# Performance work log

Measured on AMD Instinct MI355X. Metric: run time of the kernel, lower is better.

## Reference

```python
import jax, jax.numpy as jnp
import numpy as np

D_MODEL = 1024
N_HEADS = 16
D_HEAD = D_MODEL // N_HEADS


def setup_inputs() -> dict:
    key = jax.random.key(0)
    k1, k2, k3 = jax.random.split(key, 3)
    B, T = 4, 2048
    x = jax.random.normal(k1, (B, T, D_MODEL), dtype=jnp.float32)
    # torch Linear(d, 3d, bias=False): y = x @ W.T ; we store W already transposed -> [d, 3d]
    w_qkv = jax.random.normal(k2, (D_MODEL, 3 * D_MODEL), dtype=jnp.float32) * (D_MODEL ** -0.5)
    w_proj = jax.random.normal(k3, (D_MODEL, D_MODEL), dtype=jnp.float32) * (D_MODEL ** -0.5)
    return {"x": x, "w_qkv": w_qkv, "w_proj": w_proj}


def reference(x, w_qkv, w_proj):
    B, T, C = x.shape
    H, Dh = N_HEADS, D_HEAD
    qkv = (x @ w_qkv).reshape(B, T, 3, H, Dh)
    q = jnp.transpose(qkv[:, :, 0], (0, 2, 1, 3))  # [B,H,T,Dh]
    k = jnp.transpose(qkv[:, :, 1], (0, 2, 1, 3))
    v = jnp.transpose(qkv[:, :, 2], (0, 2, 1, 3))
    scale = 1.0 / jnp.sqrt(jnp.asarray(Dh, dtype=x.dtype))
    att = jnp.einsum('bhqd,bhkd->bhqk', q, k) * scale  # [B,H,T,T]
    causal = jnp.tril(jnp.ones((T, T), dtype=bool))
    att = jnp.where(causal[None, None], att, jnp.asarray(-jnp.inf, dtype=att.dtype))
    att = jax.nn.softmax(att, axis=-1)
    y = jnp.einsum('bhqk,bhkd->bhqd', att, v)          # [B,H,T,Dh]
    y = jnp.transpose(y, (0, 2, 1, 3)).reshape(B, T, C)
    return y @ w_proj
```

## Files before the change

kernel.cpp:

```cpp
#include <hip/hip_runtime.h>
#include <hip/hip_bf16.h>
#include <cmath>

#define T_SEQ 2048
#define NHEADS 16
#define DHEAD 64
#define DMODEL 1024
#define CQKV 3072

typedef __attribute__((ext_vector_type(8))) short short8;
typedef __attribute__((ext_vector_type(8))) __bf16 bf16x8;
typedef __attribute__((ext_vector_type(4))) float floatx4;

#define LDS_CAST(p) ((__attribute__((address_space(3))) void*)(p))
#define GLB_CAST(p) ((const __attribute__((address_space(1))) void*)(p))

static __device__ __forceinline__ floatx4 mfma_bf16(short8 a, short8 b, floatx4 c) {
  return __builtin_amdgcn_mfma_f32_16x16x32_bf16(
      __builtin_bit_cast(bf16x8, a), __builtin_bit_cast(bf16x8, b), c, 0, 0, 0);
}

static __device__ __forceinline__ short f2bf(float f) {
  union { float f; unsigned u; } x; x.f = f;
  unsigned r = x.u + 0x7FFFu + ((x.u >> 16) & 1u);
  return (short)(r >> 16);
}

static __device__ __forceinline__ float bf2f(short s) {
  return __builtin_bit_cast(float, ((unsigned)(unsigned short)s) << 16);
}

static __device__ __forceinline__ float exp2_(float x) {
#if __has_builtin(__builtin_amdgcn_exp2f)
  return __builtin_amdgcn_exp2f(x);
#else
  return exp2f(x);
#endif
}

static __device__ __forceinline__ bool sniff_is_bf16(const unsigned* __restrict__ x) {
  int cnt = 0;
#pragma unroll
  for (int i = 0; i < 32; ++i) {
    unsigned e = (x[i] >> 7) & 0xFFu;
    cnt += (e >= 0x70u && e <= 0x8Fu) ? 1 : 0;
  }
  return cnt >= 16;
}

static __device__ __forceinline__ short8 load8f32(const char* p, size_t idx) {
  const float4* f = (const float4*)(p + idx * 4);
  float4 a = f[0], b = f[1];
  short8 r;
  r[0] = f2bf(a.x); r[1] = f2bf(a.y); r[2] = f2bf(a.z); r[3] = f2bf(a.w);
  r[4] = f2bf(b.x); r[5] = f2bf(b.y); r[6] = f2bf(b.z); r[7] = f2bf(b.w);
  return r;
}

__global__ __launch_bounds__(256) void conv_x(const char* __restrict__ x,
                                              short* __restrict__ o, int n,
                                              const unsigned* __restrict__ xs) {
  const bool isbf = sniff_is_bf16(xs);
  const int i = (blockIdx.x * 256 + threadIdx.x) * 8;
  if (i >= n) return;
  if (isbf) *(short8*)(o + i) = *(const short8*)((const short*)x + i);
  else      *(short8*)(o + i) = load8f32(x, (size_t)i);
}

__global__ __launch_bounds__(256) void tpose(const char* __restrict__ w,
                                             short* __restrict__ wt, int K, int N,
                                             const unsigned* __restrict__ xs) {
  const bool isbf = sniff_is_bf16(xs);
  __shared__ short tile[32][33];
  const int n0 = blockIdx.x * 32, k0 = blockIdx.y * 32;
  const int tx = threadIdx.x & 31, ty = threadIdx.x >> 5;
#pragma unroll
  for (int i = 0; i < 4; ++i) {
    const int r = ty * 4 + i;
    const size_t off = (size_t)(k0 + r) * N + n0 + tx;
    tile[r][tx] = isbf ? ((const short*)w)[off] : f2bf(((const float*)w)[off]);
  }
  __syncthreads();
#pragma unroll
  for (int i = 0; i < 4; ++i) {
    const int r = ty * 4 + i;
    wt[(size_t)(n0 + r) * K + k0 + tx] = tile[tx][r];
  }
}

__global__ __launch_bounds__(256) void gemm128(const short* __restrict__ A,
                                               const short* __restrict__ Bt,
                                               void* __restrict__ C,
                                               short* __restrict__ C2,
                                               int M, int N, int K, int mode,
                                               const unsigned* __restrict__ xs) {
  const bool out_f32 = (mode == 1) ? !sniff_is_bf16(xs) : false;

  __shared__ short as[128 * 64];
  __shared__ short bs[128 * 64];
  const int tid = threadIdx.x;
  const int wid = tid >> 6, lane = tid & 63;
  const int quad = lane >> 4, l16 = lane & 15;
  const int wm = wid >> 1, wn = wid & 1;
  const int m0 = blockIdx.y * 128, n0 = blockIdx.x * 128;

  const int srl = lane >> 3;
  const int sch = ((lane & 7) ^ srl) * 8;

  const floatx4 zero4 = {0.f, 0.f, 0.f, 0.f};
  floatx4 acc[4][4];
#pragma unroll
  for (int i = 0; i < 4; ++i)
#pragma unroll
    for (int j = 0; j < 4; ++j) acc[i][j] = zero4;

  for (int kt = 0; kt < K; kt += 64) {
    __syncthreads();
#pragma unroll
    for (int i = 0; i < 4; ++i) {
      const int row = wid * 32 + i * 8;
      const short* ga = A + (size_t)(m0 + row + srl) * K + kt + sch;
      const short* gb = Bt + (size_t)(n0 + row + srl) * K + kt + sch;
      __builtin_amdgcn_global_load_lds(GLB_CAST(ga), LDS_CAST(as + row * 64), 16, 0, 0);
      __builtin_amdgcn_global_load_lds(GLB_CAST(gb), LDS_CAST(bs + row * 64), 16, 0, 0);
    }
    __syncthreads();

#pragma unroll
    for (int kc = 0; kc < 2; ++kc) {
      const int slot = ((kc * 4 + quad) ^ (l16 & 7)) * 8;
      short8 afr[4], bfr[4];
#pragma unroll
      for (int mt = 0; mt < 4; ++mt)
        afr[mt] = *(const short8*)&as[(wm * 64 + mt * 16 + l16) * 64 + slot];
#pragma unroll
      for (int nt = 0; nt < 4; ++nt)
        bfr[nt] = *(const short8*)&bs[(wn * 64 + nt * 16 + l16) * 64 + slot];
#pragma unroll
      for (int mt = 0; mt < 4; ++mt)
#pragma unroll
        for (int nt = 0; nt < 4; ++nt)
          acc[mt][nt] = mfma_bf16(afr[mt], bfr[nt], acc[mt][nt]);
    }
  }

  const int row0 = m0 + wm * 64 + quad * 4;
  const int col0 = n0 + wn * 64 + l16;
  if (mode == 2 && n0 >= 2048) {
#pragma unroll
    for (int mt = 0; mt < 4; ++mt)
#pragma unroll
      for (int nt = 0; nt < 4; ++nt)
#pragma unroll
        for (int r = 0; r < 4; ++r) {
          const int row = row0 + mt * 16 + r;
          const int col = col0 + nt * 16;
          const int d = col & 63, hh = (col >> 6) - 32;
          const int bb = row >> 11, t = row & 2047;
          C2[((size_t)(bb * 16 + hh) * 64 + d) * T_SEQ + t] = f2bf(acc[mt][nt][r]);
        }
  } else {
    const int outN = (mode == 2) ? 2048 : N;
#pragma unroll
    for (int mt = 0; mt < 4; ++mt)
#pragma unroll
      for (int nt = 0; nt < 4; ++nt)
#pragma unroll
        for (int r = 0; r < 4; ++r) {
          const size_t off = (size_t)(row0 + mt * 16 + r) * outN + col0 + nt * 16;
          if (out_f32) ((float*)C)[off] = acc[mt][nt][r];
          else         ((short*)C)[off] = f2bf(acc[mt][nt][r]);
        }
  }
}

__global__ __launch_bounds__(256) void attn(const short* __restrict__ qk,
                                            const short* __restrict__ vT,
                                            short* __restrict__ y) {
  __shared__ short ks[64 * 64];
  __shared__ short vs[64 * 64];
  __shared__ short ps[4][16][72];
  const int tid = threadIdx.x;
  const int wid = tid >> 6, lane = tid & 63;
  const int quad = lane >> 4, l16 = lane & 15;
  const int b = blockIdx.x >> 4, h = blockIdx.x & 15;
  const int q0 = ((int)gridDim.y - 1 - (int)blockIdx.y) * 64;
  const int qw0 = q0 + wid * 16;

  const short* qbase = qk + (size_t)b * T_SEQ * 2048 + h * DHEAD;
  const short* kbase = qbase + DMODEL;
  const short* vtb = vT + (size_t)(b * NHEADS + h) * DHEAD * T_SEQ;
  const float SC = 0.18033688011112042f;

  short8 aq[2];
#pragma unroll
  for (int kc = 0; kc < 2; ++kc) {
    short8 raw = *(const short8*)(qbase + (size_t)(qw0 + l16) * 2048 + kc * 32 + quad * 8);
#pragma unroll
    for (int j = 0; j < 8; ++j) aq[kc][j] = f2bf(bf2f(raw[j]) * SC);
  }

  const floatx4 zero4 = {0.f, 0.f, 0.f, 0.f};
  floatx4 o[4], lacc = zero4;
#pragma unroll
  for (int i = 0; i < 4; ++i) o[i] = zero4;
  const short8 ones8 = {0x3F80, 0x3F80, 0x3F80, 0x3F80, 0x3F80, 0x3F80, 0x3F80, 0x3F80};

  const int srl = lane >> 3;
  const int sch = ((lane & 7) ^ srl) * 8;

  const int kend = q0 + 64;
  for (int kt = 0; kt < kend; kt += 64) {
    __syncthreads();
#pragma unroll
    for (int i = 0; i < 2; ++i) {
      const int row = i * 32 + wid * 8 + srl;
      const short* gk = kbase + (size_t)(kt + row) * 2048 + sch;
      const short* gv = vtb + (size_t)row * T_SEQ + kt + sch;
      __builtin_amdgcn_global_load_lds(GLB_CAST(gk), LDS_CAST(ks + (i * 32 + wid * 8) * 64), 16, 0, 0);
      __builtin_amdgcn_global_load_lds(GLB_CAST(gv), LDS_CAST(vs + (i * 32 + wid * 8) * 64), 16, 0, 0);
    }
    __syncthreads();

    floatx4 s[4];
#pragma unroll
    for (int nt = 0; nt < 4; ++nt) {
      s[nt] = zero4;
#pragma unroll
      for (int kc = 0; kc < 2; ++kc) {
        const int slot = ((kc * 4 + quad) ^ (l16 & 7)) * 8;
        const short8 bk = *(const short8*)&ks[(nt * 16 + l16) * 64 + slot];
        s[nt] = mfma_bf16(aq[kc], bk, s[nt]);
      }
    }

    const bool full = (kt + 63 <= qw0);
#pragma unroll
    for (int nt = 0; nt < 4; ++nt)
#pragma unroll
      for (int r = 0; r < 4; ++r) {
        float p = exp2_(s[nt][r]);
        if (!full) {
          const int key = kt + nt * 16 + l16;
          const int q = qw0 + quad * 4 + r;
          p = (key <= q) ? p : 0.f;
        }
        s[nt][r] = p;
      }

#pragma unroll
    for (int nt = 0; nt < 4; ++nt)
#pragma unroll
      for (int r = 0; r < 4; ++r)
        ps[wid][quad * 4 + r][nt * 16 + l16] = f2bf(s[nt][r]);

#pragma unroll
    for (int kc = 0; kc < 2; ++kc) {
      const short8 ap = *(const short8*)&ps[wid][l16][kc * 32 + quad * 8];
      lacc = mfma_bf16(ap, ones8, lacc);
#pragma unroll
      for (int d4 = 0; d4 < 4; ++d4) {
        const int slot = ((kc * 4 + quad) ^ (l16 & 7)) * 8;
        const short8 bv = *(const short8*)&vs[(d4 * 16 + l16) * 64 + slot];
        o[d4] = mfma_bf16(ap, bv, o[d4]);
      }
    }
  }

  floatx4 inv;
#pragma unroll
  for (int r = 0; r < 4; ++r) inv[r] = 1.0f / lacc[r];
#pragma unroll
  for (int d4 = 0; d4 < 4; ++d4)
#pragma unroll
    for (int r = 0; r < 4; ++r) {
      const int q = qw0 + quad * 4 + r;
      y[(size_t)(b * T_SEQ + q) * DMODEL + h * DHEAD + d4 * 16 + l16] =
          f2bf(o[d4][r] * inv[r]);
    }
}

extern "C" void kernel_launch(void* const* d_in, const int* in_sizes, int n_in,
                              void* d_out, int out_size, void* d_ws, size_t ws_size,
                              hipStream_t stream) {
  const char* x = (const char*)d_in[0];
  const char* w_qkv = (const char*)d_in[1];
  const char* w_proj = (const char*)d_in[2];
  const unsigned* xs = (const unsigned*)d_in[0];

  short* qk = (short*)d_ws;
  short* vTb = qk + (size_t)8192 * 2048;
  short* wqkvT = vTb + (size_t)64 * 64 * 2048;
  short* wprojT = wqkvT + (size_t)3072 * 1024;
  short* xbf = wprojT + (size_t)1024 * 1024;
  short* ybuf = xbf;

  conv_x<<<8192 * 1024 / (256 * 8), 256, 0, stream>>>(x, xbf, 8192 * 1024, xs);
  {
    dim3 g1(3072 / 32, 1024 / 32);
    tpose<<<g1, 256, 0, stream>>>(w_qkv, wqkvT, 1024, 3072, xs);
    dim3 g2(1024 / 32, 1024 / 32);
    tpose<<<g2, 256, 0, stream>>>(w_proj, wprojT, 1024, 1024, xs);
  }
  {
    dim3 grid(3072 / 128, 8192 / 128);
    gemm128<<<grid, 256, 0, stream>>>(xbf, wqkvT, qk, vTb, 8192, 3072, 1024, 2, xs);
  }
  {
    dim3 grid(4 * NHEADS, T_SEQ / 64);
    attn<<<grid, 256, 0, stream>>>(qk, vTb, ybuf);
  }
  {
    dim3 grid(1024 / 128, 8192 / 128);
    gemm128<<<grid, 256, 0, stream>>>(ybuf, wprojT, d_out, nullptr, 8192, 1024, 1024, 1, xs);
  }
}
```

Baseline: 265.1 us.

## Replace 128x128 GEMM with double-buffered 256x256 tile, 8-wave pipelined kernel

The QKV and output-projection GEMMs move from a 128x128 tile, 4-wave kernel to a 256x256 tile, 8-wave kernel. The new kernel double-buffers LDS and overlaps global-to-LDS staging of the next K-tiles with the MFMA quadrants of the current one, using explicit barriers, vmcnt waits and s_setprio. It also remaps block IDs (a stride-8 interleave) to improve L2 reuse. The larger tile reduces global traffic per FLOP but uses 128KB of LDS and more registers. It also cuts the grid to 384 and 128 blocks, which may underfill the 256 CUs, especially for the projection GEMM.

```diff
diff --git a/kernel.cpp b/kernel.cpp
--- a/kernel.cpp
+++ b/kernel.cpp
@@ -88,7 +88,7 @@
   }
 }
 
-__global__ __launch_bounds__(256) void gemm128(const short* __restrict__ A,
+__global__ __launch_bounds__(512) void gemm256(const short* __restrict__ A,
                                                const short* __restrict__ Bt,
                                                void* __restrict__ C,
                                                short* __restrict__ C2,
@@ -96,82 +96,168 @@
                                                const unsigned* __restrict__ xs) {
   const bool out_f32 = (mode == 1) ? !sniff_is_bf16(xs) : false;
 
-  __shared__ short as[128 * 64];
-  __shared__ short bs[128 * 64];
+  __shared__ short as[2][256 * 64];
+  __shared__ short bs[2][256 * 64];
   const int tid = threadIdx.x;
   const int wid = tid >> 6, lane = tid & 63;
   const int quad = lane >> 4, l16 = lane & 15;
-  const int wm = wid >> 1, wn = wid & 1;
-  const int m0 = blockIdx.y * 128, n0 = blockIdx.x * 128;
+  const int wm = wid >> 2, wn = wid & 3;
+
+  const int gx = (int)gridDim.x;
+  const int nwg = gx * (int)gridDim.y;
+  int bid = (int)blockIdx.y * gx + (int)blockIdx.x;
+  bid = (bid & 7) * (nwg >> 3) + (bid >> 3);
+  const int m0 = (bid / gx) * 256;
+  const int n0 = (bid % gx) * 256;
 
   const int srl = lane >> 3;
   const int sch = ((lane & 7) ^ srl) * 8;
+  const int NT = K >> 6;
+
+#define STAGE_A(t, h, b)                                                          \
+  do {                                                                            \
+    const int kt_ = (t) << 6;                                                     \
+    _Pragma("unroll") for (int j_ = 0; j_ < 2; ++j_) {                            \
+      const int row_ = (h) * 128 + j_ * 64 + wid * 8;                             \
+      const short* g_ = A + (size_t)(m0 + row_ + srl) * K + kt_ + sch;            \
+      __builtin_amdgcn_global_load_lds(GLB_CAST(g_), LDS_CAST(&as[(b)][row_ * 64]), 16, 0, 0); \
+    }                                                                             \
+  } while (0)
+
+#define STAGE_B(t, h, b)                                                          \
+  do {                                                                            \
+    const int kt_ = (t) << 6;                                                     \
+    _Pragma("unroll") for (int j_ = 0; j_ < 2; ++j_) {                            \
+      const int row_ = (h) * 128 + j_ * 64 + wid * 8;                             \
+      const short* g_ = Bt + (size_t)(n0 + row_ + srl) * K + kt_ + sch;           \
+      __builtin_amdgcn_global_load_lds(GLB_CAST(g_), LDS_CAST(&bs[(b)][row_ * 64]), 16, 0, 0); \
+    }                                                                             \
+  } while (0)
+
+#define SLOT_(kc) ((((kc) * 4 + quad) ^ (l16 & 7)) * 8)
+
+#define LOAD_A(dst, mh, b)                                                        \
+  do {                                                                            \
+    _Pragma("unroll") for (int mf_ = 0; mf_ < 4; ++mf_)                           \
+    _Pragma("unroll") for (int kc_ = 0; kc_ < 2; ++kc_)                           \
+      dst[mf_][kc_] = *(const short8*)&as[(b)][(wm * 128 + (mh) * 64 + mf_ * 16 + l16) * 64 + SLOT_(kc_)]; \
+  } while (0)
+
+#define LOAD_B(dst, nh, b)                                                        \
+  do {                                                                            \
+    _Pragma("unroll") for (int nf_ = 0; nf_ < 2; ++nf_)                           \
+    _Pragma("unroll") for (int kc_ = 0; kc_ < 2; ++kc_)                           \
+      dst[nf_][kc_] = *(const short8*)&bs[(b)][(wn * 64 + (nh) * 32 + nf_ * 16 + l16) * 64 + SLOT_(kc_)]; \
+  } while (0)
+
+#define QMFMA(afrag, bfrag, mh, nh)                                               \
+  do {                                                                            \
+    __builtin_amdgcn_s_setprio(1);                                                \
+    _Pragma("unroll") for (int mf_ = 0; mf_ < 4; ++mf_)                           \
+    _Pragma("unroll") for (int nf_ = 0; nf_ < 2; ++nf_)                           \
+    _Pragma("unroll") for (int kc_ = 0; kc_ < 2; ++kc_)                           \
+      acc[(mh) * 4 + mf_][(nh) * 2 + nf_] =                                       \
+          mfma_bf16(afrag[mf_][kc_], bfrag[nf_][kc_], acc[(mh) * 4 + mf_][(nh) * 2 + nf_]); \
+    __builtin_amdgcn_s_setprio(0);                                                \
+  } while (0)
+
+#define BAR_()                                                                    \
+  do {                                                                            \
+    __builtin_amdgcn_sched_barrier(0);                                            \
+    __builtin_amdgcn_s_barrier();                                                 \
+    __builtin_amdgcn_sched_barrier(0);                                            \
+  } while (0)
+
+#define WAITV_(n)                                                                 \
+  do {                                                                            \
+    asm volatile("s_waitcnt vmcnt(" #n ")" ::: "memory");                         \
+    __builtin_amdgcn_sched_barrier(0);                                            \
+  } while (0)
 
   const floatx4 zero4 = {0.f, 0.f, 0.f, 0.f};
-  floatx4 acc[4][4];
-#pragma unroll
-  for (int i = 0; i < 4; ++i)
+  floatx4 acc[8][4];
+#pragma unroll
+  for (int i = 0; i < 8; ++i)
 #pragma unroll
     for (int j = 0; j < 4; ++j) acc[i][j] = zero4;
 
-  for (int kt = 0; kt < K; kt += 64) {
-    __syncthreads();
-#pragma unroll
-    for (int i = 0; i < 4; ++i) {
-      const int row = wid * 32 + i * 8;
-      const short* ga = A + (size_t)(m0 + row + srl) * K + kt + sch;
-      const short* gb = Bt + (size_t)(n0 + row + srl) * K + kt + sch;
-      __builtin_amdgcn_global_load_lds(GLB_CAST(ga), LDS_CAST(as + row * 64), 16, 0, 0);
-      __builtin_amdgcn_global_load_lds(GLB_CAST(gb), LDS_CAST(bs + row * 64), 16, 0, 0);
-    }
-    __syncthreads();
-
-#pragma unroll
-    for (int kc = 0; kc < 2; ++kc) {
-      const int slot = ((kc * 4 + quad) ^ (l16 & 7)) * 8;
-      short8 afr[4], bfr[4];
-#pragma unroll
-      for (int mt = 0; mt < 4; ++mt)
-        afr[mt] = *(const short8*)&as[(wm * 64 + mt * 16 + l16) * 64 + slot];
-#pragma unroll
-      for (int nt = 0; nt < 4; ++nt)
-        bfr[nt] = *(const short8*)&bs[(wn * 64 + nt * 16 + l16) * 64 + slot];
-#pragma unroll
-      for (int mt = 0; mt < 4; ++mt)
-#pragma unroll
-        for (int nt = 0; nt < 4; ++nt)
-          acc[mt][nt] = mfma_bf16(afr[mt], bfr[nt], acc[mt][nt]);
-    }
-  }
-
-  const int row0 = m0 + wm * 64 + quad * 4;
+  STAGE_B(0, 0, 0); STAGE_B(0, 1, 0);
+  STAGE_A(0, 0, 0); STAGE_A(0, 1, 0);
+  STAGE_B(1, 0, 1); STAGE_B(1, 1, 1);
+  WAITV_(4);
+  BAR_();
+
+  short8 afr[4][2], bf0[2][2], bf1[2][2];
+
+  for (int t = 0; t < NT; ++t) {
+    const int cb = t & 1, nb = cb ^ 1;
+    const int tA = (t + 1 < NT) ? t + 1 : NT - 1;
+    const int tB = (t + 2 < NT) ? t + 2 : NT - 1;
+
+    LOAD_A(afr, 0, cb);
+    LOAD_B(bf0, 0, cb);
+    STAGE_A(tA, 0, nb);
+    BAR_();
+    QMFMA(afr, bf0, 0, 0);
+    BAR_();
+
+    LOAD_B(bf1, 1, cb);
+    STAGE_A(tA, 1, nb);
+    BAR_();
+    QMFMA(afr, bf1, 0, 1);
+    BAR_();
+
+    LOAD_A(afr, 1, cb);
+    STAGE_B(tB, 0, cb);
+    BAR_();
+    QMFMA(afr, bf1, 1, 1);
+    BAR_();
+
+    STAGE_B(tB, 1, cb);
+    WAITV_(4);
+    BAR_();
+    QMFMA(afr, bf0, 1, 0);
+    BAR_();
+  }
+  asm volatile("s_waitcnt vmcnt(0)" ::: "memory");
+  __builtin_amdgcn_sched_barrier(0);
+
+  const int row0 = m0 + wm * 128 + quad * 4;
   const int col0 = n0 + wn * 64 + l16;
   if (mode == 2 && n0 >= 2048) {
 #pragma unroll
-    for (int mt = 0; mt < 4; ++mt)
-#pragma unroll
-      for (int nt = 0; nt < 4; ++nt)
+    for (int mi = 0; mi < 8; ++mi)
+#pragma unroll
+      for (int ni = 0; ni < 4; ++ni)
 #pragma unroll
         for (int r = 0; r < 4; ++r) {
-          const int row = row0 + mt * 16 + r;
-          const int col = col0 + nt * 16;
+          const int row = row0 + mi * 16 + r;
+          const int col = col0 + ni * 16;
           const int d = col & 63, hh = (col >> 6) - 32;
-          const int bb = row >> 11, t = row & 2047;
-          C2[((size_t)(bb * 16 + hh) * 64 + d) * T_SEQ + t] = f2bf(acc[mt][nt][r]);
+          const int bb = row >> 11, tq = row & 2047;
+          C2[((size_t)(bb * 16 + hh) * 64 + d) * T_SEQ + tq] = f2bf(acc[mi][ni][r]);
         }
   } else {
     const int outN = (mode == 2) ? 2048 : N;
 #pragma unroll
-    for (int mt = 0; mt < 4; ++mt)
-#pragma unroll
-      for (int nt = 0; nt < 4; ++nt)
+    for (int mi = 0; mi < 8; ++mi)
+#pragma unroll
+      for (int ni = 0; ni < 4; ++ni)
 #pragma unroll
         for (int r = 0; r < 4; ++r) {
-          const size_t off = (size_t)(row0 + mt * 16 + r) * outN + col0 + nt * 16;
-          if (out_f32) ((float*)C)[off] = acc[mt][nt][r];
-          else         ((short*)C)[off] = f2bf(acc[mt][nt][r]);
+          const size_t off = (size_t)(row0 + mi * 16 + r) * outN + col0 + ni * 16;
+          if (out_f32) ((float*)C)[off] = acc[mi][ni][r];
+          else         ((short*)C)[off] = f2bf(acc[mi][ni][r]);
         }
   }
+#undef STAGE_A
+#undef STAGE_B
+#undef SLOT_
+#undef LOAD_A
+#undef LOAD_B
+#undef QMFMA
+#undef BAR_
+#undef WAITV_
 }
 
 __global__ __launch_bounds__(256) void attn(const short* __restrict__ qk,
@@ -303,15 +389,15 @@
     tpose<<<g2, 256, 0, stream>>>(w_proj, wprojT, 1024, 1024, xs);
   }
   {
-    dim3 grid(3072 / 128, 8192 / 128);
-    gemm128<<<grid, 256, 0, stream>>>(xbf, wqkvT, qk, vTb, 8192, 3072, 1024, 2, xs);
+    dim3 grid(3072 / 256, 8192 / 256);
+    gemm256<<<grid, 512, 0, stream>>>(xbf, wqkvT, qk, vTb, 8192, 3072, 1024, 2, xs);
   }
   {
     dim3 grid(4 * NHEADS, T_SEQ / 64);
     attn<<<grid, 256, 0, stream>>>(qk, vTb, ybuf);
   }
   {
-    dim3 grid(1024 / 128, 8192 / 128);
-    gemm128<<<grid, 256, 0, stream>>>(ybuf, wprojT, d_out, nullptr, 8192, 1024, 1024, 1, xs);
-  }
-}
+    dim3 grid(1024 / 256, 8192 / 256);
+    gemm256<<<grid, 512, 0, stream>>>(ybuf, wprojT, d_out, nullptr, 8192, 1024, 1024, 1, xs);
+  }
+}
```

New measurement: 283.9 us. 1.07x slower.
